# Performance work log

Hardware: AMD Instinct MI355X
Metric: run time of the kernel (lower is better)

## Reference

```python
import jax, jax.numpy as jnp
import numpy as np

DIM = 384
HEADS = 12
HEAD_DIM = DIM // HEADS
WIN = (2, 7, 7)
NW_TOK = WIN[0] * WIN[1] * WIN[2]  # 98
SCALE = HEAD_DIM ** -0.5


def _relative_position_index():
    d = np.arange(WIN[0]); h = np.arange(WIN[1]); w = np.arange(WIN[2])
    coords = np.stack(np.meshgrid(d, h, w, indexing='ij'))  # [3,D,H,W]
    cf = coords.reshape(3, -1)  # [3, NW_TOK]
    rel = cf[:, :, None] - cf[:, None, :]  # [3, N, N]
    rel = rel.transpose(1, 2, 0).astype(np.int64)
    rel[:, :, 0] += WIN[0] - 1
    rel[:, :, 1] += WIN[1] - 1
    rel[:, :, 2] += WIN[2] - 1
    rel[:, :, 0] *= (2 * WIN[1] - 1) * (2 * WIN[2] - 1)
    rel[:, :, 1] *= 2 * WIN[2] - 1
    return rel.sum(-1)  # [NW_TOK, NW_TOK]


def setup_inputs() -> dict:
    key = jax.random.key(0)
    ks = jax.random.split(key, 6)
    B_, N = 1024, NW_TOK + 1
    nW = 64
    table_len = (2 * WIN[0] - 1) * (2 * WIN[1] - 1) * (2 * WIN[2] - 1)  # 507
    x = jax.random.normal(ks[0], (B_, N, DIM), dtype=jnp.float32)
    mask = jax.random.normal(ks[1], (nW, NW_TOK, NW_TOK), dtype=jnp.float32)
    W_qkv = jax.random.normal(ks[2], (DIM, 3 * DIM), dtype=jnp.float32) * 0.02
    rpb_table = jax.random.normal(ks[3], (table_len, HEADS), dtype=jnp.float32) * 0.02
    W_proj = jax.random.normal(ks[4], (DIM, DIM), dtype=jnp.float32) * 0.02
    b_proj = jnp.zeros((DIM,), dtype=jnp.float32)
    rpi = jnp.asarray(_relative_position_index(), dtype=jnp.int32)
    return {"x": x, "mask": mask, "W_qkv": W_qkv, "rpb_table": rpb_table,
            "W_proj": W_proj, "b_proj": b_proj, "rpi": rpi}


def reference(x, mask, W_qkv, rpb_table, W_proj, b_proj, rpi):
    B_, N, C = x.shape
    qkv = (x @ W_qkv).reshape(B_, N, 3, HEADS, HEAD_DIM)
    q, k, v = qkv[:, :, 0], qkv[:, :, 1], qkv[:, :, 2]  # [B_, N, H, hd]
    attn = jnp.einsum('bnhd,bmhd->bhnm', q * SCALE, k)  # [B_, H, N, N]
    # gathered relative position bias over non-class tokens, zero-padded for class token
    bias = rpb_table[rpi.reshape(-1)].reshape(NW_TOK, NW_TOK, HEADS).transpose(2, 0, 1)
    bias_full = jnp.pad(bias, ((0, 0), (1, 0), (1, 0)))  # [H, N, N]
    attn = attn + bias_full[None]
    nW = mask.shape[0]
    mask_full = jnp.pad(mask, ((0, 0), (1, 0), (1, 0)))  # [nW, N, N]
    attn = attn.reshape(B_ // nW, nW, HEADS, N, N) + mask_full[None, :, None]
    attn = attn.reshape(B_, HEADS, N, N)
    attn = jax.nn.softmax(attn, axis=-1)
    out = jnp.einsum('bhnm,bmhd->bnhd', attn, v).reshape(B_, N, C)
    out = out @ W_proj + b_proj
    return out[:, 1:], out[:, :1]
```

## Files before the change

kernel.cpp:

```cpp
#include <hip/hip_runtime.h>
#include <hip/hip_bf16.h>
#include <cstddef>
#include <cstdint>


using bf16 = __hip_bfloat16;
typedef short v8s __attribute__((ext_vector_type(8)));
typedef short v4s __attribute__((ext_vector_type(4)));
typedef float v4f __attribute__((ext_vector_type(4)));

static constexpr int    NTOK   = 99;
static constexpr int    CDIM   = 384;
static constexpr int    NHEAD  = 12;
static constexpr int    NROWS  = 101376;
static constexpr size_t PLANE  = (size_t)NROWS * 32;
static constexpr float  SCALEF = 0.17677669529663687f;

__device__ __forceinline__ v4f mfma16x16x32(v8s a, v8s b, v4f c) {
  return __builtin_amdgcn_mfma_f32_16x16x32_bf16(a, b, c, 0, 0, 0);
}
__device__ __forceinline__ short f2bf(float f) {
  bf16 h = __float2bfloat16(f);
  return *reinterpret_cast<short*>(&h);
}
__device__ __forceinline__ float bf2f(short s) {
  bf16 h = *reinterpret_cast<bf16*>(&s);
  return __bfloat162float(h);
}

#if defined(__has_builtin)
#if __has_builtin(__builtin_amdgcn_global_load_lds)
#define HAS_GLL 1
#endif
#endif
#ifndef HAS_GLL
#define HAS_GLL 0
#endif

__device__ __forceinline__ void gload_lds16(const bf16* gsrc, bf16* ldst, int lane) {
#if HAS_GLL
  __builtin_amdgcn_global_load_lds(
      (const __attribute__((address_space(1))) void*)gsrc,
      (__attribute__((address_space(3))) void*)ldst, 16, 0, 0);
#else
  *(v8s*)(ldst + lane * 8) = *(const v8s*)gsrc;
#endif
}

static constexpr size_t WT_QKV_OFF = 0;
static constexpr size_t WT_P_OFF   = 884736;
static constexpr size_t BIAS_OFF   = 884736 + 294912;
static constexpr size_t COMMON_END = 1650096;
static constexpr size_t O_WS_OFF   = COMMON_END;
static constexpr size_t WS_MID     = O_WS_OFF + (size_t)NROWS * 384 * 2;
static constexpr size_t BMF_OFF    = COMMON_END;
static constexpr size_t BMF_BYTES  = (size_t)64 * NHEAD * 7 * 7 * 64 * 4 * 2;
static constexpr size_t QKV_OFF    = BMF_OFF + BMF_BYTES;
static constexpr size_t WS_FULL    = QKV_OFF + (size_t)NROWS * 1152 * 2;
static constexpr size_t XB_OFF     = WS_FULL;
static constexpr size_t WS_FULL2   = XB_OFF + (size_t)NROWS * 384 * 2;

static constexpr int PREP_BASE = 1152 * 384 + 384 * 384 + NHEAD * 99 * 99;
static constexpr int PREP_BMF2 = 64 * 112 * 112;
static constexpr int PREP_XB   = NROWS * 384 / 8;

__global__ void prep_kernel(const float* __restrict__ Wqkv, const float* __restrict__ Wproj,
                            const float* __restrict__ rpb,  const int* __restrict__ rpi,
                            const float* __restrict__ mask, const float* __restrict__ x,
                            bf16* __restrict__ WtQKV, bf16* __restrict__ WtP,
                            float* __restrict__ BIAS, bf16* __restrict__ BMF,
                            bf16* __restrict__ xb, int do_bmf, int do_xb)
{
  int idx = blockIdx.x * 256 + threadIdx.x;
  if (idx < 1152 * 384) {
    int c = idx / 384, k = idx - c * 384;
    WtQKV[idx] = __float2bfloat16(Wqkv[k * 1152 + c]);
  } else if (idx < 1152 * 384 + 384 * 384) {
    int j = idx - 1152 * 384;
    int c = j / 384, k = j - c * 384;
    WtP[j] = __float2bfloat16(Wproj[k * 384 + c]);
  } else if (idx < PREP_BASE) {
    int j = idx - (1152 * 384 + 384 * 384);
    int h = j / (99 * 99), r = j % (99 * 99);
    int nn = r / 99, mm = r % 99;
    float v = 0.f;
    if (nn > 0 && mm > 0) v = rpb[rpi[(nn - 1) * 98 + (mm - 1)] * NHEAD + h];
    BIAS[j] = v;
  } else if (do_bmf && idx < PREP_BASE + PREP_BMF2) {
    int j2  = idx - PREP_BASE;
    int col = j2 % 112;
    int r2  = j2 / 112;
    int row = r2 % 112;
    int wi  = r2 / 112;
    int w = row >> 4, g = (row >> 2) & 3, jj = row & 3;
    int t = col >> 4, li = col & 15, lane = g * 16 + li;
    bool in = (row >= 1 && row <= 98 && col >= 1 && col <= 98);
    int tix = 0; float mval = 0.f;
    if (in) {
      tix  = rpi[(row - 1) * 98 + (col - 1)];
      mval = mask[((size_t)wi * 98 + (row - 1)) * 98 + (col - 1)];
    }
    size_t base = (((size_t)wi * NHEAD * 7 + w) * 7 + t) * 256 + lane * 4 + jj;
    #pragma unroll
    for (int h = 0; h < NHEAD; ++h) {
      float v = in ? (rpb[tix * NHEAD + h] + mval) : 0.f;
      BMF[base + (size_t)h * 12544] = __float2bfloat16(v);
    }
  } else if (do_xb && idx >= PREP_BASE + PREP_BMF2 &&
             idx < PREP_BASE + PREP_BMF2 + PREP_XB) {
    int j3 = idx - (PREP_BASE + PREP_BMF2);
    size_t off = (size_t)j3 * 8;
    v4f x0 = *(const v4f*)(x + off);
    v4f x1 = *(const v4f*)(x + off + 4);
    v8s f;
    #pragma unroll
    for (int j = 0; j < 4; ++j) { f[j] = f2bf(x0[j]); f[j + 4] = f2bf(x1[j]); }
    *(v8s*)(xb + off) = f;
  }
}

static constexpr int Q2_BUF  = 40960;
static constexpr int Q2_AOFF = 24576;
static constexpr int CSTG_LD = 104;

__global__ __launch_bounds__(512)
void k_qkv2(const bf16* __restrict__ xb, const bf16* __restrict__ WtQKV,
            bf16* __restrict__ qkv2)
{
  __shared__ __align__(16) char smem[2 * Q2_BUF];
  bf16* C_stg = (bf16*)(smem);

  const int tid  = threadIdx.x;
  const int wave = tid >> 6;
  const int wm   = wave >> 2;
  const int wn   = wave & 3;
  const int lane = tid & 63;
  const int g    = lane >> 4;
  const int li   = lane & 15;
  const int tile = (blockIdx.x & 7) * 594 + (blockIdx.x >> 3);
  const int R0   = (tile / 6) * 128;
  const int CN   = (tile % 6) * 192;

  v4f acc[4][3];
  #pragma unroll
  for (int mi = 0; mi < 4; ++mi)
    #pragma unroll
    for (int ni = 0; ni < 3; ++ni) acc[mi][ni] = (v4f){0.f, 0.f, 0.f, 0.f};

  auto stage = [&](int kc, int buf) {
    const int k0 = kc * 64;
    bf16* Bl = (bf16*)(smem + buf * Q2_BUF);
    bf16* Al = (bf16*)(smem + buf * Q2_BUF + Q2_AOFF);
    #pragma unroll
    for (int p = 0; p < 3; ++p) {
      int q = wave * 3 + p;
      int row = q * 8 + (lane >> 3);
      int c = (lane & 7) ^ (row & 7);
      gload_lds16(WtQKV + (size_t)(CN + row) * 384 + k0 + c * 8, Bl + q * 512, lane);
    }
    #pragma unroll
    for (int p = 0; p < 2; ++p) {
      int q = wave * 2 + p;
      int row = q * 8 + (lane >> 3);
      int c = (lane & 7) ^ (row & 7);
      gload_lds16(xb + (size_t)(R0 + row) * 384 + k0 + c * 8, Al + q * 512, lane);
    }
  };

  stage(0, 0);
  for (int kc = 0; kc < 6; ++kc) {
    if (kc < 5) {
      stage(kc + 1, (kc + 1) & 1);
      asm volatile("s_waitcnt vmcnt(5)" ::: "memory");
    } else {
      asm volatile("s_waitcnt vmcnt(0)" ::: "memory");
    }
    __builtin_amdgcn_s_barrier();
    __builtin_amdgcn_sched_barrier(0);
    const bf16* Bl = (const bf16*)(smem + (kc & 1) * Q2_BUF);
    const bf16* Al = (const bf16*)(smem + (kc & 1) * Q2_BUF + Q2_AOFF);
    #pragma unroll
    for (int ks = 0; ks < 2; ++ks) {
      v8s af[4], bfr[3];
      #pragma unroll
      for (int mi = 0; mi < 4; ++mi) {
        int arow = wm * 64 + mi * 16 + li;
        int sc   = (4 * ks + g) ^ (arow & 7);
        af[mi] = *(const v8s*)(Al + arow * 64 + sc * 8);
      }
      #pragma unroll
      for (int ni = 0; ni < 3; ++ni) {
        int brow = wn * 48 + ni * 16 + li;
        int sc   = (4 * ks + g) ^ (brow & 7);
        bfr[ni] = *(const v8s*)(Bl + brow * 64 + sc * 8);
      }
      #pragma unroll
      for (int mi = 0; mi < 4; ++mi)
        #pragma unroll
        for (int ni = 0; ni < 3; ++ni)
          acc[mi][ni] = mfma16x16x32(af[mi], bfr[ni], acc[mi][ni]);
    }
    __builtin_amdgcn_sched_barrier(0);
    __builtin_amdgcn_s_barrier();
  }

  const float scale = (CN < 384) ? SCALEF : 1.f;
  const int r_ep = tid >> 2, d8 = tid & 3;
  #pragma unroll
  for (int half = 0; half < 2; ++half) {
    __syncthreads();
    if ((wn >> 1) == half) {
      #pragma unroll
      for (int mi = 0; mi < 4; ++mi)
        #pragma unroll
        for (int ni = 0; ni < 3; ++ni)
          #pragma unroll
          for (int j = 0; j < 4; ++j)
            C_stg[(wm * 64 + mi * 16 + g * 4 + j) * CSTG_LD + (wn & 1) * 48 + ni * 16 + li] =
                __float2bfloat16(acc[mi][ni][j] * scale);
    }
    __syncthreads();
    #pragma unroll
    for (int cidx = 0; cidx < 3; ++cidx) {
      int c_global = CN + half * 96 + cidx * 32;
      int seg = c_global / 384, hh = (c_global % 384) >> 5;
      bf16* plane = qkv2 + (size_t)(hh * 3 + seg) * PLANE;
      v8s val = *(const v8s*)(C_stg + r_ep * CSTG_LD + cidx * 32 + d8 * 8);
      *(v8s*)(plane + (size_t)(R0 + r_ep) * 32 + d8 * 8) = val;
    }
  }
}

static constexpr int GQB_OFF  = 0;
static constexpr int GQA_OFF  = 24576;
static constexpr int GQ_LDS2  = GQA_OFF + 128 * 72 * 2;

__global__ __launch_bounds__(512)
void k_qkv(const float* __restrict__ x, const bf16* __restrict__ WtQKV,
           bf16* __restrict__ qkv2)
{
  __shared__ __align__(16) char smem[GQ_LDS2];
  bf16* B_lds = (bf16*)(smem + GQB_OFF);
  bf16* A_lds = (bf16*)(smem + GQA_OFF);
  bf16* C_stg = (bf16*)(smem);

  const int tid  = threadIdx.x;
  const int wave = tid >> 6;
  const int wm   = wave >> 2;
  const int wn   = wave & 3;
  const int lane = tid & 63;
  const int g    = lane >> 4;
  const int li   = lane & 15;
  const int tile = (blockIdx.x & 7) * 594 + (blockIdx.x >> 3);
  const int R0   = (tile / 6) * 128;
  const int CN   = (tile % 6) * 192;

  const int arr = tid >> 3, ak8 = tid & 7;

  v4f acc[4][3];
  #pragma unroll
  for (int mi = 0; mi < 4; ++mi)
    #pragma unroll
    for (int ni = 0; ni < 3; ++ni) acc[mi][ni] = (v4f){0.f, 0.f, 0.f, 0.f};

  v4f areg[2][2];
  auto load_areg = [&](int kc) {
    const int k0 = kc * 64;
    #pragma unroll
    for (int p = 0; p < 2; ++p) {
      const float* src = x + (size_t)(R0 + arr + p * 64) * 384 + k0 + ak8 * 8;
      areg[p][0] = *(const v4f*)(src);
      areg[p][1] = *(const v4f*)(src + 4);
    }
  };
  auto write_alds = [&]() {
    #pragma unroll
    for (int p = 0; p < 2; ++p) {
      v8s f;
      #pragma unroll
      for (int j = 0; j < 4; ++j) { f[j] = f2bf(areg[p][0][j]); f[j + 4] = f2bf(areg[p][1][j]); }
      *(v8s*)(A_lds + (arr + p * 64) * 72 + ak8 * 8) = f;
    }
  };

  load_areg(0);

  for (int kc = 0; kc < 6; ++kc) {
    const int k0 = kc * 64;
    write_alds();
    #pragma unroll
    for (int p = 0; p < 3; ++p) {
      int q   = wave * 3 + p;
      int row = q * 8 + (lane >> 3);
      int c   = (lane & 7) ^ (row & 7);
      const bf16* gsrc = WtQKV + (size_t)(CN + row) * 384 + k0 + c * 8;
      gload_lds16(gsrc, B_lds + q * 512, lane);
    }
    if (kc < 5) load_areg(kc + 1);
    __syncthreads();
    #pragma unroll
    for (int ks = 0; ks < 2; ++ks) {
      v8s af[4], bfr[3];
      #pragma unroll
      for (int mi = 0; mi < 4; ++mi)
        af[mi] = *(const v8s*)(A_lds + (wm * 64 + mi * 16 + li) * 72 + ks * 32 + g * 8);
      #pragma unroll
      for (int ni = 0; ni < 3; ++ni) {
        int brow = wn * 48 + ni * 16 + li;
        int sc   = (g + 4 * ks) ^ (brow & 7);
        bfr[ni]  = *(const v8s*)(B_lds + brow * 64 + sc * 8);
      }
      #pragma unroll
      for (int mi = 0; mi < 4; ++mi)
        #pragma unroll
        for (int ni = 0; ni < 3; ++ni)
          acc[mi][ni] = mfma16x16x32(af[mi], bfr[ni], acc[mi][ni]);
    }
    __syncthreads();
  }

  const float scale = (CN < 384) ? SCALEF : 1.f;
  const int r_ep = tid >> 2, d8 = tid & 3;
  #pragma unroll
  for (int half = 0; half < 2; ++half) {
    __syncthreads();
    if ((wn >> 1) == half) {
      #pragma unroll
      for (int mi = 0; mi < 4; ++mi)
        #pragma unroll
        for (int ni = 0; ni < 3; ++ni)
          #pragma unroll
          for (int j = 0; j < 4; ++j)
            C_stg[(wm * 64 + mi * 16 + g * 4 + j) * CSTG_LD + (wn & 1) * 48 + ni * 16 + li] =
                __float2bfloat16(acc[mi][ni][j] * scale);
    }
    __syncthreads();
    #pragma unroll
    for (int cidx = 0; cidx < 3; ++cidx) {
      int c_global = CN + half * 96 + cidx * 32;
      int seg = c_global / 384, hh = (c_global % 384) >> 5;
      bf16* plane = qkv2 + (size_t)(hh * 3 + seg) * PLANE;
      v8s val = *(const v8s*)(C_stg + r_ep * CSTG_LD + cidx * 32 + d8 * 8);
      *(v8s*)(plane + (size_t)(R0 + r_ep) * 32 + d8 * 8) = val;
    }
  }
}

static constexpr int A_VT_LD = 136;
static constexpr int A_P_LD  = 136;
static constexpr int A_OFF_V = 0;
static constexpr int A_OFF_P = A_OFF_V + 32 * A_VT_LD * 2;
static constexpr int A_LDS   = A_OFF_P + 112 * A_P_LD * 2;

__global__ __launch_bounds__(448)
void k_attn(const bf16* __restrict__ BMF, bf16* __restrict__ qkv2)
{
  __shared__ __align__(16) char smem[A_LDS];
  bf16* vT_lds = (bf16*)(smem + A_OFF_V);
  bf16* P_lds  = (bf16*)(smem + A_OFF_P);

  const int b    = blockIdx.x;
  const int h0   = blockIdx.y * 3;
  const int tid  = threadIdx.x;
  const int wave = tid >> 6;
  const int lane = tid & 63;
  const int g    = lane >> 4;
  const int li   = lane & 15;
  const int wi   = b & 63;

  for (int z = tid; z < 32 * 29; z += 448)
    vT_lds[(z / 29) * A_VT_LD + 99 + (z % 29)] = __float2bfloat16(0.f);
  for (int z = tid; z < 112 * 29; z += 448)
    P_lds[(z / 29) * A_P_LD + 99 + (z % 29)] = __float2bfloat16(0.f);

  const int r = tid >> 2, l4 = tid & 3;
  const size_t voff = ((size_t)b * NTOK + ((r > 98) ? 98 : r)) * 32 + l4 * 8;

  const int qrow = (16 * wave + li > 98) ? 98 : 16 * wave + li;
  const size_t qoff = ((size_t)b * NTOK + qrow) * 32 + g * 8;
  size_t koff[7];
  #pragma unroll
  for (int t = 0; t < 7; ++t) {
    int krow = 16 * t + li; if (krow > 98) krow = 98;
    koff[t] = ((size_t)b * NTOK + krow) * 32 + g * 8;
  }

  {
    v8s pv = *(const v8s*)(qkv2 + (size_t)(h0 * 3 + 2) * PLANE + voff);
    if (r < NTOK) {
      #pragma unroll
      for (int e = 0; e < 8; ++e)
        *(short*)(vT_lds + (l4 * 8 + e) * A_VT_LD + r) = pv[e];
    }
  }
  __syncthreads();

  v4f oaccs[3][2];

  #pragma unroll
  for (int hi = 0; hi < 3; ++hi) {
    const int h = h0 + hi;
    v8s nv;
    if (hi < 2) nv = *(const v8s*)(qkv2 + (size_t)(h * 3 + 5) * PLANE + voff);

    const bf16* kp = qkv2 + (size_t)(h * 3 + 1) * PLANE;
    v8s kf[7];
    #pragma unroll
    for (int t = 0; t < 7; ++t) kf[t] = *(const v8s*)(kp + koff[t]);
    v8s qf = *(const v8s*)(qkv2 + (size_t)(h * 3 + 0) * PLANE + qoff);

    const bf16* bmb = BMF + ((size_t)((wi * NHEAD + h) * 7 + wave) * 7) * 256;
    v4s bmr[7];
    #pragma unroll
    for (int t = 0; t < 7; ++t)
      bmr[t] = *(const v4s*)(bmb + t * 256 + lane * 4);

    v4f sacc[7];
    #pragma unroll
    for (int t = 0; t < 7; ++t) {
      v4f z = (v4f){0.f, 0.f, 0.f, 0.f};
      sacc[t] = mfma16x16x32(qf, kf[t], z);
    }
    #pragma unroll
    for (int t = 0; t < 7; ++t) {
      int col = 16 * t + li;
      #pragma unroll
      for (int j = 0; j < 4; ++j) {
        float s = sacc[t][j];
        if (col >= NTOK) s = -1e30f;
        else             s += bf2f(bmr[t][j]);
        sacc[t][j] = s;
      }
    }
    float linv[4];
    #pragma unroll
    for (int j = 0; j < 4; ++j) {
      float m = -1e30f;
      #pragma unroll
      for (int t = 0; t < 7; ++t) m = fmaxf(m, sacc[t][j]);
      m = fmaxf(m, __shfl_xor(m, 1));
      m = fmaxf(m, __shfl_xor(m, 2));
      m = fmaxf(m, __shfl_xor(m, 4));
      m = fmaxf(m, __shfl_xor(m, 8));
      float l = 0.f;
      #pragma unroll
      for (int t = 0; t < 7; ++t) {
        float p = __expf(sacc[t][j] - m);
        sacc[t][j] = p;
        l += p;
      }
      l += __shfl_xor(l, 1);
      l += __shfl_xor(l, 2);
      l += __shfl_xor(l, 4);
      l += __shfl_xor(l, 8);
      linv[j] = 1.f / l;
      int row = 16 * wave + g * 4 + j;
      #pragma unroll
      for (int t = 0; t < 7; ++t) {
        int col = 16 * t + li;
        if (col < NTOK) P_lds[row * A_P_LD + col] = __float2bfloat16(sacc[t][j]);
      }
    }
    v4f oacc[2];
    oacc[0] = (v4f){0.f, 0.f, 0.f, 0.f};
    oacc[1] = (v4f){0.f, 0.f, 0.f, 0.f};
    #pragma unroll
    for (int ks = 0; ks < 4; ++ks) {
      v8s ap = *(const v8s*)(P_lds + (16 * wave + li) * A_P_LD + ks * 32 + g * 8);
      #pragma unroll
      for (int t = 0; t < 2; ++t) {
        v8s bv = *(const v8s*)(vT_lds + (16 * t + li) * A_VT_LD + ks * 32 + g * 8);
        oacc[t] = mfma16x16x32(ap, bv, oacc[t]);
      }
    }
    #pragma unroll
    for (int t = 0; t < 2; ++t)
      #pragma unroll
      for (int j = 0; j < 4; ++j)
        oaccs[hi][t][j] = oacc[t][j] * linv[j];

    __syncthreads();
    if (hi < 2) {
      if (r < NTOK) {
        #pragma unroll
        for (int e = 0; e < 8; ++e)
          *(short*)(vT_lds + (l4 * 8 + e) * A_VT_LD + r) = nv[e];
      }
      __syncthreads();
    }
  }

  #pragma unroll
  for (int hi = 0; hi < 3; ++hi) {
    bf16* oplane = qkv2 + (size_t)((h0 + hi) * 3) * PLANE;
    #pragma unroll
    for (int t = 0; t < 2; ++t)
      #pragma unroll
      for (int j = 0; j < 4; ++j) {
        int row = 16 * wave + g * 4 + j;
        if (row < NTOK)
          oplane[((size_t)b * NTOK + row) * 32 + 16 * t + li] =
              __float2bfloat16(oaccs[hi][t][j]);
      }
  }
}

__global__ __launch_bounds__(512)
void k2_proj2(const bf16* __restrict__ O_src, const bf16* __restrict__ WtP,
              const float* __restrict__ bproj, float* __restrict__ out)
{
  __shared__ __align__(16) char smem[2 * Q2_BUF];

  const int tid  = threadIdx.x;
  const int wave = tid >> 6;
  const int wm   = wave >> 2;
  const int wn   = wave & 3;
  const int lane = tid & 63;
  const int g    = lane >> 4;
  const int li   = lane & 15;
  const int tile = (blockIdx.x & 7) * 198 + (blockIdx.x >> 3);
  const int R0   = (tile >> 1) * 128;
  const int CN   = (tile & 1) * 192;

  v4f acc[4][3];
  #pragma unroll
  for (int mi = 0; mi < 4; ++mi)
    #pragma unroll
    for (int ni = 0; ni < 3; ++ni) acc[mi][ni] = (v4f){0.f, 0.f, 0.f, 0.f};

  auto stage = [&](int kc, int buf) {
    const int k0 = kc * 64;
    bf16* Wl = (bf16*)(smem + buf * Q2_BUF);
    bf16* Ol = (bf16*)(smem + buf * Q2_BUF + Q2_AOFF);
    #pragma unroll
    for (int p = 0; p < 3; ++p) {
      int q = wave * 3 + p;
      int row = q * 8 + (lane >> 3);
      int c = (lane & 7) ^ (row & 7);
      gload_lds16(WtP + (size_t)(CN + row) * CDIM + k0 + c * 8, Wl + q * 512, lane);
    }
    #pragma unroll
    for (int p = 0; p < 2; ++p) {
      int q = wave * 2 + p;
      int row = q * 8 + (lane >> 3);
      int c = (lane & 7) ^ (row & 7);
      int kk = k0 + c * 8, hh = kk >> 5, d = kk & 31;
      gload_lds16(O_src + (size_t)(hh * 3) * PLANE + (size_t)(R0 + row) * 32 + d,
                  Ol + q * 512, lane);
    }
  };

  stage(0, 0);
  for (int kc = 0; kc < 6; ++kc) {
    if (kc < 5) {
      stage(kc + 1, (kc + 1) & 1);
      asm volatile("s_waitcnt vmcnt(5)" ::: "memory");
    } else {
      asm volatile("s_waitcnt vmcnt(0)" ::: "memory");
    }
    __builtin_amdgcn_s_barrier();
    __builtin_amdgcn_sched_barrier(0);
    const bf16* Wl = (const bf16*)(smem + (kc & 1) * Q2_BUF);
    const bf16* Ol = (const bf16*)(smem + (kc & 1) * Q2_BUF + Q2_AOFF);
    #pragma unroll
    for (int ks = 0; ks < 2; ++ks) {
      v8s af[4], bfr[3];
      #pragma unroll
      for (int mi = 0; mi < 4; ++mi) {
        int arow = wm * 64 + mi * 16 + li;
        int sc   = (4 * ks + g) ^ (arow & 7);
        af[mi] = *(const v8s*)(Ol + arow * 64 + sc * 8);
      }
      #pragma unroll
      for (int ni = 0; ni < 3; ++ni) {
        int brow = wn * 48 + ni * 16 + li;
        int sc   = (4 * ks + g) ^ (brow & 7);
        bfr[ni] = *(const v8s*)(Wl + brow * 64 + sc * 8);
      }
      #pragma unroll
      for (int mi = 0; mi < 4; ++mi)
        #pragma unroll
        for (int ni = 0; ni < 3; ++ni)
          acc[mi][ni] = mfma16x16x32(af[mi], bfr[ni], acc[mi][ni]);
    }
    __builtin_amdgcn_sched_barrier(0);
    __builtin_amdgcn_s_barrier();
  }

  const size_t OUT2 = (size_t)1024 * 98 * CDIM;
  #pragma unroll
  for (int mi = 0; mi < 4; ++mi)
    #pragma unroll
    for (int ni = 0; ni < 3; ++ni) {
      int col = CN + wn * 48 + ni * 16 + li;
      float bb = bproj[col];
      #pragma unroll
      for (int j = 0; j < 4; ++j) {
        int rr = R0 + wm * 64 + mi * 16 + g * 4 + j;
        int b = rr / 99, n = rr - b * 99;
        float v = acc[mi][ni][j] + bb;
        if (n == 0) out[OUT2 + (size_t)b * CDIM + col] = v;
        else        out[((size_t)b * 98 + (n - 1)) * CDIM + col] = v;
      }
    }
}

static constexpr int K2_LD   = 72;
static constexpr int K2_OFFW = 0;
static constexpr int K2_OFFO = 192 * K2_LD * 2;
static constexpr int K2_LDS  = K2_OFFO + 128 * K2_LD * 2;

__global__ __launch_bounds__(512)
void k2_proj(const bf16* __restrict__ O_src, const bf16* __restrict__ WtP,
             const float* __restrict__ bproj, float* __restrict__ out)
{
  __shared__ __align__(16) char smem[K2_LDS];
  bf16* W_lds = (bf16*)(smem + K2_OFFW);
  bf16* O_lds = (bf16*)(smem + K2_OFFO);

  const int tid  = threadIdx.x;
  const int wave = tid >> 6;
  const int wm   = wave >> 2;
  const int wn   = wave & 3;
  const int lane = tid & 63;
  const int g    = lane >> 4;
  const int li   = lane & 15;
  const int tile = (blockIdx.x & 7) * 198 + (blockIdx.x >> 3);
  const int R0   = (tile >> 1) * 128;
  const int CN   = (tile & 1) * 192;

  v4f acc[4][3];
  #pragma unroll
  for (int mi = 0; mi < 4; ++mi)
    #pragma unroll
    for (int ni = 0; ni < 3; ++ni) acc[mi][ni] = (v4f){0.f, 0.f, 0.f, 0.f};

  for (int kc = 0; kc < 6; ++kc) {
    const int k0 = kc * 64;
    #pragma unroll
    for (int p = 0; p < 3; ++p) {
      int it = tid + p * 512, rr = it >> 3, k8 = it & 7;
      *(v8s*)(W_lds + rr * K2_LD + k8 * 8) =
          *(const v8s*)(WtP + (size_t)(CN + rr) * CDIM + k0 + k8 * 8);
    }
    #pragma unroll
    for (int p = 0; p < 2; ++p) {
      int it = tid + p * 512, rr = it >> 3, k8 = it & 7;
      *(v8s*)(O_lds + rr * K2_LD + k8 * 8) =
          *(const v8s*)(O_src + (size_t)(R0 + rr) * 384 + k0 + k8 * 8);
    }
    __syncthreads();
    #pragma unroll
    for (int ks = 0; ks < 2; ++ks) {
      v8s af[4], bfr[3];
      #pragma unroll
      for (int mi = 0; mi < 4; ++mi)
        af[mi] = *(const v8s*)(O_lds + (wm * 64 + mi * 16 + li) * K2_LD + ks * 32 + g * 8);
      #pragma unroll
      for (int ni = 0; ni < 3; ++ni)
        bfr[ni] = *(const v8s*)(W_lds + (wn * 48 + ni * 16 + li) * K2_LD + ks * 32 + g * 8);
      #pragma unroll
      for (int mi = 0; mi < 4; ++mi)
        #pragma unroll
        for (int ni = 0; ni < 3; ++ni)
          acc[mi][ni] = mfma16x16x32(af[mi], bfr[ni], acc[mi][ni]);
    }
    __syncthreads();
  }

  const size_t OUT2 = (size_t)1024 * 98 * CDIM;
  #pragma unroll
  for (int mi = 0; mi < 4; ++mi)
    #pragma unroll
    for (int ni = 0; ni < 3; ++ni) {
      int col = CN + wn * 48 + ni * 16 + li;
      float bb = bproj[col];
      #pragma unroll
      for (int j = 0; j < 4; ++j) {
        int rr = R0 + wm * 64 + mi * 16 + g * 4 + j;
        int b = rr / 99, n = rr - b * 99;
        float v = acc[mi][ni][j] + bb;
        if (n == 0) out[OUT2 + (size_t)b * CDIM + col] = v;
        else        out[((size_t)b * 98 + (n - 1)) * CDIM + col] = v;
      }
    }
}

static constexpr int QK_LD = 40;
static constexpr int VT_LD = 136;
static constexpr int P_LD  = 136;
static constexpr int WS_LD = 104;
static constexpr int K1_OFF_Q = 0;
static constexpr int K1_OFF_K = K1_OFF_Q + 112 * QK_LD * 2;
static constexpr int K1_OFF_V = K1_OFF_K + 112 * QK_LD * 2;
static constexpr int K1_OFF_P = K1_OFF_V + 32  * VT_LD * 2;
static constexpr int K1_OFF_W = K1_OFF_P + 112 * P_LD  * 2;
static constexpr int K1_LDS   = K1_OFF_W + 96 * WS_LD * 2;

__global__ __launch_bounds__(512)
void k1_attn(const float* __restrict__ x, const float* __restrict__ mask,
             const float* __restrict__ BIAS, const bf16* __restrict__ WtQKV,
             bf16* __restrict__ O_ws)
{
  __shared__ __align__(16) char smem[K1_LDS];
  bf16* q_lds  = (bf16*)(smem + K1_OFF_Q);
  bf16* k_lds  = (bf16*)(smem + K1_OFF_K);
  bf16* vT_lds = (bf16*)(smem + K1_OFF_V);
  bf16* P_lds  = (bf16*)(smem + K1_OFF_P);
  bf16* w_lds  = (bf16*)(smem + K1_OFF_W);

  const int b    = blockIdx.x;
  const int tid  = threadIdx.x;
  const int wave = tid >> 6;
  const int lane = tid & 63;
  const int g    = lane >> 4;
  const int li   = lane & 15;
  const int wi   = b & 63;

  v8s afr[12];
  if (wave < 7) {
    int arow = 16 * wave + li; if (arow > 98) arow = 98;
    const float* xb = x + ((size_t)b * NTOK + arow) * CDIM + g * 8;
    #pragma unroll
    for (int s = 0; s < 12; ++s) {
      v4f x0 = *(const v4f*)(xb + s * 32);
      v4f x1 = *(const v4f*)(xb + s * 32 + 4);
      v8s f;
      #pragma unroll
      for (int j = 0; j < 4; ++j) { f[j] = f2bf(x0[j]); f[j + 4] = f2bf(x1[j]); }
      afr[s] = f;
    }
  }

  for (int h = 0; h < NHEAD; ++h) {
    v4f qacc[6];
    #pragma unroll
    for (int t = 0; t < 6; ++t) qacc[t] = (v4f){0.f, 0.f, 0.f, 0.f};
    #pragma unroll
    for (int c4 = 0; c4 < 4; ++c4) {
      for (int idx = tid; idx < 96 * 12; idx += 512) {
        int rr = idx / 12, ch = idx - rr * 12;
        int cg = (rr < 32) ? (h * 32 + rr)
               : (rr < 64) ? (CDIM + h * 32 + rr - 32)
                           : (2 * CDIM + h * 32 + rr - 64);
        *(v8s*)(w_lds + rr * WS_LD + ch * 8) =
            *(const v8s*)(WtQKV + (size_t)cg * CDIM + c4 * 96 + ch * 8);
      }
      __syncthreads();
      if (wave < 7) {
        #pragma unroll
        for (int ss = 0; ss < 3; ++ss) {
          const int s = c4 * 3 + ss;
          #pragma unroll
          for (int t = 0; t < 6; ++t) {
            v8s bw = *(const v8s*)(w_lds + (16 * t + li) * WS_LD + ss * 32 + g * 8);
            qacc[t] = mfma16x16x32(afr[s], bw, qacc[t]);
          }
        }
      }
      __syncthreads();
    }
    if (wave < 7) {
      #pragma unroll
      for (int t = 0; t < 6; ++t) {
        #pragma unroll
        for (int j = 0; j < 4; ++j) {
          int row = 16 * wave + g * 4 + j;
          int col = 16 * (t & 1) + li;
          float v = qacc[t][j];
          if (t < 2)      q_lds[row * QK_LD + col] = __float2bfloat16(v * SCALEF);
          else if (t < 4) k_lds[row * QK_LD + col] = __float2bfloat16(v);
          else            vT_lds[col * VT_LD + row] = __float2bfloat16(v);
        }
      }
    }
    vT_lds[(tid >> 4) * VT_LD + 112 + (tid & 15)] = __float2bfloat16(0.f);
    __syncthreads();

    if (wave < 7) {
      v8s aq = *(const v8s*)(q_lds + (16 * wave + li) * QK_LD + g * 8);
      v4f sacc[7];
      #pragma unroll
      for (int t = 0; t < 7; ++t) {
        v8s bk = *(const v8s*)(k_lds + (16 * t + li) * QK_LD + g * 8);
        v4f z = (v4f){0.f, 0.f, 0.f, 0.f};
        sacc[t] = mfma16x16x32(aq, bk, z);
      }
      #pragma unroll
      for (int t = 0; t < 7; ++t) {
        int col = 16 * t + li;
        #pragma unroll
        for (int j = 0; j < 4; ++j) {
          int row = 16 * wave + g * 4 + j;
          float s = sacc[t][j];
          if (col >= NTOK) s = -1e30f;
          else if (row < NTOK) {
            s += BIAS[(h * NTOK + row) * NTOK + col];
            if (row > 0 && col > 0)
              s += mask[((size_t)wi * 98 + (row - 1)) * 98 + (col - 1)];
          }
          sacc[t][j] = s;
        }
      }
      float linv[4];
      #pragma unroll
      for (int j = 0; j < 4; ++j) {
        float m = -1e30f;
        #pragma unroll
        for (int t = 0; t < 7; ++t) m = fmaxf(m, sacc[t][j]);
        m = fmaxf(m, __shfl_xor(m, 1));
        m = fmaxf(m, __shfl_xor(m, 2));
        m = fmaxf(m, __shfl_xor(m, 4));
        m = fmaxf(m, __shfl_xor(m, 8));
        float l = 0.f;
        #pragma unroll
        for (int t = 0; t < 7; ++t) {
          float p = __expf(sacc[t][j] - m);
          sacc[t][j] = p;
          l += p;
        }
        l += __shfl_xor(l, 1);
        l += __shfl_xor(l, 2);
        l += __shfl_xor(l, 4);
        l += __shfl_xor(l, 8);
        linv[j] = 1.f / l;
        int row = 16 * wave + g * 4 + j;
        #pragma unroll
        for (int t = 0; t < 7; ++t)
          P_lds[row * P_LD + 16 * t + li] = __float2bfloat16(sacc[t][j]);
        P_lds[row * P_LD + 112 + li] = __float2bfloat16(0.f);
      }
      v4f oacc[2];
      oacc[0] = (v4f){0.f, 0.f, 0.f, 0.f};
      oacc[1] = (v4f){0.f, 0.f, 0.f, 0.f};
      #pragma unroll
      for (int ks = 0; ks < 4; ++ks) {
        v8s ap = *(const v8s*)(P_lds + (16 * wave + li) * P_LD + ks * 32 + g * 8);
        #pragma unroll
        for (int t = 0; t < 2; ++t) {
          v8s bv = *(const v8s*)(vT_lds + (16 * t + li) * VT_LD + ks * 32 + g * 8);
          oacc[t] = mfma16x16x32(ap, bv, oacc[t]);
        }
      }
      #pragma unroll
      for (int t = 0; t < 2; ++t) {
        #pragma unroll
        for (int j = 0; j < 4; ++j) {
          int row = 16 * wave + g * 4 + j;
          if (row < NTOK)
            O_ws[((size_t)b * 99 + row) * CDIM + h * 32 + 16 * t + li] =
                __float2bfloat16(oacc[t][j] * linv[j]);
        }
      }
    }
    __syncthreads();
  }
}

static constexpr int M_O_LD = 392;
static constexpr int M_OFF_O = 0;
static constexpr int M_OFF_Q = M_OFF_O + 99  * M_O_LD * 2;
static constexpr int M_OFF_K = M_OFF_Q + 112 * QK_LD * 2;
static constexpr int M_OFF_V = M_OFF_K + 112 * QK_LD * 2;
static constexpr int M_OFF_P = M_OFF_V + 32  * VT_LD * 2;
static constexpr int M_OFF_W = M_OFF_P + 112 * P_LD  * 2;
static constexpr int M_LDS   = M_OFF_W + 96 * WS_LD * 2;

__global__ __launch_bounds__(512)
void fused_mono(const float* __restrict__ x, const float* __restrict__ mask,
                const float* __restrict__ bproj, const float* __restrict__ BIAS,
                const bf16* __restrict__ WtQKV, const bf16* __restrict__ WtP,
                float* __restrict__ out)
{
  __shared__ __align__(16) char smem[M_LDS];
  bf16* O_lds  = (bf16*)(smem + M_OFF_O);
  bf16* q_lds  = (bf16*)(smem + M_OFF_Q);
  bf16* k_lds  = (bf16*)(smem + M_OFF_K);
  bf16* vT_lds = (bf16*)(smem + M_OFF_V);
  bf16* P_lds  = (bf16*)(smem + M_OFF_P);
  bf16* w_lds  = (bf16*)(smem + M_OFF_W);

  const int b    = blockIdx.x;
  const int tid  = threadIdx.x;
  const int wave = tid >> 6;
  const int lane = tid & 63;
  const int g    = lane >> 4;
  const int li   = lane & 15;
  const int wi   = b & 63;

  v8s afr[12];
  if (wave < 7) {
    int arow = 16 * wave + li; if (arow > 98) arow = 98;
    const float* xb = x + ((size_t)b * NTOK + arow) * CDIM + g * 8;
    #pragma unroll
    for (int s = 0; s < 12; ++s) {
      v4f x0 = *(const v4f*)(xb + s * 32);
      v4f x1 = *(const v4f*)(xb + s * 32 + 4);
      v8s f;
      #pragma unroll
      for (int j = 0; j < 4; ++j) { f[j] = f2bf(x0[j]); f[j + 4] = f2bf(x1[j]); }
      afr[s] = f;
    }
  }

  for (int h = 0; h < NHEAD; ++h) {
    v4f qacc[6];
    #pragma unroll
    for (int t = 0; t < 6; ++t) qacc[t] = (v4f){0.f, 0.f, 0.f, 0.f};
    #pragma unroll
    for (int c4 = 0; c4 < 4; ++c4) {
      for (int idx = tid; idx < 96 * 12; idx += 512) {
        int rr = idx / 12, ch = idx - rr * 12;
        int cg = (rr < 32) ? (h * 32 + rr)
               : (rr < 64) ? (CDIM + h * 32 + rr - 32)
                           : (2 * CDIM + h * 32 + rr - 64);
        *(v8s*)(w_lds + rr * WS_LD + ch * 8) =
            *(const v8s*)(WtQKV + (size_t)cg * CDIM + c4 * 96 + ch * 8);
      }
      __syncthreads();
      if (wave < 7) {
        #pragma unroll
        for (int ss = 0; ss < 3; ++ss) {
          const int s = c4 * 3 + ss;
          #pragma unroll
          for (int t = 0; t < 6; ++t) {
            v8s bw = *(const v8s*)(w_lds + (16 * t + li) * WS_LD + ss * 32 + g * 8);
            qacc[t] = mfma16x16x32(afr[s], bw, qacc[t]);
          }
        }
      }
      __syncthreads();
    }
    if (wave < 7) {
      #pragma unroll
      for (int t = 0; t < 6; ++t) {
        #pragma unroll
        for (int j = 0; j < 4; ++j) {
          int row = 16 * wave + g * 4 + j;
          int col = 16 * (t & 1) + li;
          float v = qacc[t][j];
          if (t < 2)      q_lds[row * QK_LD + col] = __float2bfloat16(v * SCALEF);
          else if (t < 4) k_lds[row * QK_LD + col] = __float2bfloat16(v);
          else            vT_lds[col * VT_LD + row] = __float2bfloat16(v);
        }
      }
    }
    vT_lds[(tid >> 4) * VT_LD + 112 + (tid & 15)] = __float2bfloat16(0.f);
    __syncthreads();

    if (wave < 7) {
      v8s aq = *(const v8s*)(q_lds + (16 * wave + li) * QK_LD + g * 8);
      v4f sacc[7];
      #pragma unroll
      for (int t = 0; t < 7; ++t) {
        v8s bk = *(const v8s*)(k_lds + (16 * t + li) * QK_LD + g * 8);
        v4f z = (v4f){0.f, 0.f, 0.f, 0.f};
        sacc[t] = mfma16x16x32(aq, bk, z);
      }
      #pragma unroll
      for (int t = 0; t < 7; ++t) {
        int col = 16 * t + li;
        #pragma unroll
        for (int j = 0; j < 4; ++j) {
          int row = 16 * wave + g * 4 + j;
          float s = sacc[t][j];
          if (col >= NTOK) s = -1e30f;
          else if (row < NTOK) {
            s += BIAS[(h * NTOK + row) * NTOK + col];
            if (row > 0 && col > 0)
              s += mask[((size_t)wi * 98 + (row - 1)) * 98 + (col - 1)];
          }
          sacc[t][j] = s;
        }
      }
      float linv[4];
      #pragma unroll
      for (int j = 0; j < 4; ++j) {
        float m = -1e30f;
        #pragma unroll
        for (int t = 0; t < 7; ++t) m = fmaxf(m, sacc[t][j]);
        m = fmaxf(m, __shfl_xor(m, 1));
        m = fmaxf(m, __shfl_xor(m, 2));
        m = fmaxf(m, __shfl_xor(m, 4));
        m = fmaxf(m, __shfl_xor(m, 8));
        float l = 0.f;
        #pragma unroll
        for (int t = 0; t < 7; ++t) {
          float p = __expf(sacc[t][j] - m);
          sacc[t][j] = p;
          l += p;
        }
        l += __shfl_xor(l, 1);
        l += __shfl_xor(l, 2);
        l += __shfl_xor(l, 4);
        l += __shfl_xor(l, 8);
        linv[j] = 1.f / l;
        int row = 16 * wave + g * 4 + j;
        #pragma unroll
        for (int t = 0; t < 7; ++t)
          P_lds[row * P_LD + 16 * t + li] = __float2bfloat16(sacc[t][j]);
        P_lds[row * P_LD + 112 + li] = __float2bfloat16(0.f);
      }
      v4f oacc[2];
      oacc[0] = (v4f){0.f, 0.f, 0.f, 0.f};
      oacc[1] = (v4f){0.f, 0.f, 0.f, 0.f};
      #pragma unroll
      for (int ks = 0; ks < 4; ++ks) {
        v8s ap = *(const v8s*)(P_lds + (16 * wave + li) * P_LD + ks * 32 + g * 8);
        #pragma unroll
        for (int t = 0; t < 2; ++t) {
          v8s bv = *(const v8s*)(vT_lds + (16 * t + li) * VT_LD + ks * 32 + g * 8);
          oacc[t] = mfma16x16x32(ap, bv, oacc[t]);
        }
      }
      #pragma unroll
      for (int t = 0; t < 2; ++t) {
        #pragma unroll
        for (int j = 0; j < 4; ++j) {
          int row = 16 * wave + g * 4 + j;
          if (row < NTOK)
            O_lds[row * M_O_LD + h * 32 + 16 * t + li] =
                __float2bfloat16(oacc[t][j] * linv[j]);
        }
      }
    }
    __syncthreads();
  }

  const size_t OUT2 = (size_t)1024 * 98 * CDIM;
  const int orow_clamped = (16 * wave + li > 98) ? 98 : 16 * wave + li;
  for (int cc = 0; cc < 4; ++cc) {
    v4f pacc[6];
    #pragma unroll
    for (int t = 0; t < 6; ++t) pacc[t] = (v4f){0.f, 0.f, 0.f, 0.f};
    for (int c4 = 0; c4 < 4; ++c4) {
      for (int idx = tid; idx < 96 * 12; idx += 512) {
        int rr = idx / 12, ch = idx - rr * 12;
        *(v8s*)(w_lds + rr * WS_LD + ch * 8) =
            *(const v8s*)(WtP + ((size_t)(cc * 96 + rr)) * CDIM + c4 * 96 + ch * 8);
      }
      __syncthreads();
      if (wave < 7) {
        #pragma unroll
        for (int ss = 0; ss < 3; ++ss) {
          const int s = c4 * 3 + ss;
          v8s ao = *(const v8s*)(O_lds + orow_clamped * M_O_LD + s * 32 + g * 8);
          #pragma unroll
          for (int t = 0; t < 6; ++t) {
            v8s bw = *(const v8s*)(w_lds + (16 * t + li) * WS_LD + ss * 32 + g * 8);
            pacc[t] = mfma16x16x32(ao, bw, pacc[t]);
          }
        }
      }
      __syncthreads();
    }
    if (wave < 7) {
      #pragma unroll
      for (int t = 0; t < 6; ++t) {
        #pragma unroll
        for (int j = 0; j < 4; ++j) {
          int row = 16 * wave + g * 4 + j;
          if (row < NTOK) {
            int col = cc * 96 + 16 * t + li;
            float v = pacc[t][j] + bproj[col];
            if (row == 0) out[OUT2 + (size_t)b * CDIM + col] = v;
            else          out[((size_t)b * 98 + (row - 1)) * CDIM + col] = v;
          }
        }
      }
    }
  }
}

extern "C" void kernel_launch(void* const* d_in, const int* in_sizes, int n_in,
                              void* d_out, int out_size, void* d_ws, size_t ws_size,
                              hipStream_t stream) {
  const float* x     = (const float*)d_in[0];
  const float* mask  = (const float*)d_in[1];
  const float* Wqkv  = (const float*)d_in[2];
  const float* rpb   = (const float*)d_in[3];
  const float* Wproj = (const float*)d_in[4];
  const float* bproj = (const float*)d_in[5];
  const int*   rpi   = (const int*)d_in[6];

  bf16*  WtQKV = (bf16*)((char*)d_ws + WT_QKV_OFF);
  bf16*  WtP   = (bf16*)((char*)d_ws + WT_P_OFF);
  float* BIAS  = (float*)((char*)d_ws + BIAS_OFF);
  bf16*  BMF   = (bf16*)((char*)d_ws + BMF_OFF);
  bf16*  xbuf  = (bf16*)((char*)d_ws + XB_OFF);

  const bool full2 = (ws_size >= WS_FULL2);
  const bool full  = (ws_size >= WS_FULL);
  int prep_items = PREP_BASE;
  if (full)  prep_items += PREP_BMF2;
  if (full2) prep_items += PREP_XB;
  prep_kernel<<<(prep_items + 255) / 256, 256, 0, stream>>>(
      Wqkv, Wproj, rpb, rpi, mask, x, WtQKV, WtP, BIAS, BMF, xbuf,
      full ? 1 : 0, full2 ? 1 : 0);

  if (full) {
    bf16* qkv2 = (bf16*)((char*)d_ws + QKV_OFF);
    if (full2) k_qkv2<<<792 * 6, 512, 0, stream>>>(xbuf, WtQKV, qkv2);
    else       k_qkv<<<792 * 6, 512, 0, stream>>>(x, WtQKV, qkv2);
    k_attn<<<dim3(1024, 4), 448, 0, stream>>>(BMF, qkv2);
    k2_proj2<<<792 * 2, 512, 0, stream>>>(qkv2, WtP, bproj, (float*)d_out);
  } else if (ws_size >= WS_MID) {
    bf16* O_ws = (bf16*)((char*)d_ws + O_WS_OFF);
    k1_attn<<<1024, 512, 0, stream>>>(x, mask, BIAS, WtQKV, O_ws);
    k2_proj<<<792 * 2, 512, 0, stream>>>(O_ws, WtP, bproj, (float*)d_out);
  } else {
    fused_mono<<<1024, 512, 0, stream>>>(x, mask, bproj, BIAS, WtQKV, WtP,
                                         (float*)d_out);
  }
}
```

Before: 442.3 us.

## Prefetch next head's Q/K/V in attention kernel and fold padding mask into bias

Result: faster. 422.8 us (-4.4%).

```diff
diff --git a/kernel.cpp b/kernel.cpp
--- a/kernel.cpp
+++ b/kernel.cpp
@@ -103,7 +103,9 @@
     size_t base = (((size_t)wi * NHEAD * 7 + w) * 7 + t) * 256 + lane * 4 + jj;
     #pragma unroll
     for (int h = 0; h < NHEAD; ++h) {
-      float v = in ? (rpb[tix * NHEAD + h] + mval) : 0.f;
+      float v;
+      if (col > 98)  v = -1e30f;
+      else           v = in ? (rpb[tix * NHEAD + h] + mval) : 0.f;
       BMF[base + (size_t)h * 12544] = __float2bfloat16(v);
     }
   } else if (do_xb && idx >= PREP_BASE + PREP_BMF2 &&
@@ -360,7 +362,7 @@
   bf16* P_lds  = (bf16*)(smem + A_OFF_P);
 
   const int b    = blockIdx.x;
-  const int h0   = blockIdx.y * 3;
+  const int h0   = blockIdx.y * 6;
   const int tid  = threadIdx.x;
   const int wave = tid >> 6;
   const int lane = tid & 63;
@@ -368,46 +370,42 @@
   const int li   = lane & 15;
   const int wi   = b & 63;
 
-  for (int z = tid; z < 32 * 29; z += 448)
-    vT_lds[(z / 29) * A_VT_LD + 99 + (z % 29)] = __float2bfloat16(0.f);
-  for (int z = tid; z < 112 * 29; z += 448)
-    P_lds[(z / 29) * A_P_LD + 99 + (z % 29)] = __float2bfloat16(0.f);
-
   const int r = tid >> 2, l4 = tid & 3;
   const size_t voff = ((size_t)b * NTOK + ((r > 98) ? 98 : r)) * 32 + l4 * 8;
 
   const int qrow = (16 * wave + li > 98) ? 98 : 16 * wave + li;
   const size_t qoff = ((size_t)b * NTOK + qrow) * 32 + g * 8;
-  size_t koff[7];
+  int koff[7];
   #pragma unroll
   for (int t = 0; t < 7; ++t) {
     int krow = 16 * t + li; if (krow > 98) krow = 98;
-    koff[t] = ((size_t)b * NTOK + krow) * 32 + g * 8;
-  }
-
+    koff[t] = (b * NTOK + krow) * 32 + g * 8;
+  }
+
+  v8s pv = *(const v8s*)(qkv2 + (size_t)(h0 * 3 + 2) * PLANE + voff);
+
+  for (int z = tid; z < A_LDS / 16; z += 448)
+    *(v8s*)(smem + z * 16) = (v8s){0, 0, 0, 0, 0, 0, 0, 0};
+  __syncthreads();
+
+  if (r < NTOK) {
+    #pragma unroll
+    for (int e = 0; e < 8; ++e)
+      *(short*)(vT_lds + (l4 * 8 + e) * A_VT_LD + r) = pv[e];
+  }
+
+  v8s kf[7], qf;
   {
-    v8s pv = *(const v8s*)(qkv2 + (size_t)(h0 * 3 + 2) * PLANE + voff);
-    if (r < NTOK) {
-      #pragma unroll
-      for (int e = 0; e < 8; ++e)
-        *(short*)(vT_lds + (l4 * 8 + e) * A_VT_LD + r) = pv[e];
-    }
+    const bf16* kp = qkv2 + (size_t)(h0 * 3 + 1) * PLANE;
+    #pragma unroll
+    for (int t = 0; t < 7; ++t) kf[t] = *(const v8s*)(kp + koff[t]);
+    qf = *(const v8s*)(qkv2 + (size_t)(h0 * 3) * PLANE + qoff);
   }
   __syncthreads();
 
-  v4f oaccs[3][2];
-
   #pragma unroll
-  for (int hi = 0; hi < 3; ++hi) {
+  for (int hi = 0; hi < 6; ++hi) {
     const int h = h0 + hi;
-    v8s nv;
-    if (hi < 2) nv = *(const v8s*)(qkv2 + (size_t)(h * 3 + 5) * PLANE + voff);
-
-    const bf16* kp = qkv2 + (size_t)(h * 3 + 1) * PLANE;
-    v8s kf[7];
-    #pragma unroll
-    for (int t = 0; t < 7; ++t) kf[t] = *(const v8s*)(kp + koff[t]);
-    v8s qf = *(const v8s*)(qkv2 + (size_t)(h * 3 + 0) * PLANE + qoff);
 
     const bf16* bmb = BMF + ((size_t)((wi * NHEAD + h) * 7 + wave) * 7) * 256;
     v4s bmr[7];
@@ -421,17 +419,22 @@
       v4f z = (v4f){0.f, 0.f, 0.f, 0.f};
       sacc[t] = mfma16x16x32(qf, kf[t], z);
     }
-    #pragma unroll
-    for (int t = 0; t < 7; ++t) {
-      int col = 16 * t + li;
-      #pragma unroll
-      for (int j = 0; j < 4; ++j) {
-        float s = sacc[t][j];
-        if (col >= NTOK) s = -1e30f;
-        else             s += bf2f(bmr[t][j]);
-        sacc[t][j] = s;
-      }
-    }
+
+    v8s nv;
+    if (hi < 5) {
+      const bf16* kp = qkv2 + (size_t)((h + 1) * 3 + 1) * PLANE;
+      #pragma unroll
+      for (int t = 0; t < 7; ++t) kf[t] = *(const v8s*)(kp + koff[t]);
+      qf = *(const v8s*)(qkv2 + (size_t)((h + 1) * 3) * PLANE + qoff);
+      nv = *(const v8s*)(qkv2 + (size_t)((h + 1) * 3 + 2) * PLANE + voff);
+    }
+
+    #pragma unroll
+    for (int t = 0; t < 7; ++t)
+      #pragma unroll
+      for (int j = 0; j < 4; ++j)
+        sacc[t][j] += bf2f(bmr[t][j]);
+
     float linv[4];
     #pragma unroll
     for (int j = 0; j < 4; ++j) {
@@ -456,10 +459,8 @@
       linv[j] = 1.f / l;
       int row = 16 * wave + g * 4 + j;
       #pragma unroll
-      for (int t = 0; t < 7; ++t) {
-        int col = 16 * t + li;
-        if (col < NTOK) P_lds[row * A_P_LD + col] = __float2bfloat16(sacc[t][j]);
-      }
+      for (int t = 0; t < 7; ++t)
+        P_lds[row * A_P_LD + 16 * t + li] = __float2bfloat16(sacc[t][j]);
     }
     v4f oacc[2];
     oacc[0] = (v4f){0.f, 0.f, 0.f, 0.f};
@@ -473,26 +474,7 @@
         oacc[t] = mfma16x16x32(ap, bv, oacc[t]);
       }
     }
-    #pragma unroll
-    for (int t = 0; t < 2; ++t)
-      #pragma unroll
-      for (int j = 0; j < 4; ++j)
-        oaccs[hi][t][j] = oacc[t][j] * linv[j];
-
-    __syncthreads();
-    if (hi < 2) {
-      if (r < NTOK) {
-        #pragma unroll
-        for (int e = 0; e < 8; ++e)
-          *(short*)(vT_lds + (l4 * 8 + e) * A_VT_LD + r) = nv[e];
-      }
-      __syncthreads();
-    }
-  }
-
-  #pragma unroll
-  for (int hi = 0; hi < 3; ++hi) {
-    bf16* oplane = qkv2 + (size_t)((h0 + hi) * 3) * PLANE;
+    bf16* oplane = qkv2 + (size_t)(h * 3) * PLANE;
     #pragma unroll
     for (int t = 0; t < 2; ++t)
       #pragma unroll
@@ -500,8 +482,18 @@
         int row = 16 * wave + g * 4 + j;
         if (row < NTOK)
           oplane[((size_t)b * NTOK + row) * 32 + 16 * t + li] =
-              __float2bfloat16(oaccs[hi][t][j]);
-      }
+              __float2bfloat16(oacc[t][j] * linv[j]);
+      }
+
+    __syncthreads();
+    if (hi < 5) {
+      if (r < NTOK) {
+        #pragma unroll
+        for (int e = 0; e < 8; ++e)
+          *(short*)(vT_lds + (l4 * 8 + e) * A_VT_LD + r) = nv[e];
+      }
+      __syncthreads();
+    }
   }
 }
 
@@ -1102,7 +1094,7 @@
     bf16* qkv2 = (bf16*)((char*)d_ws + QKV_OFF);
     if (full2) k_qkv2<<<792 * 6, 512, 0, stream>>>(xbuf, WtQKV, qkv2);
     else       k_qkv<<<792 * 6, 512, 0, stream>>>(x, WtQKV, qkv2);
-    k_attn<<<dim3(1024, 4), 448, 0, stream>>>(BMF, qkv2);
+    k_attn<<<dim3(1024, 2), 448, 0, stream>>>(BMF, qkv2);
     k2_proj2<<<792 * 2, 512, 0, stream>>>(qkv2, WtP, bproj, (float*)d_out);
   } else if (ws_size >= WS_MID) {
     bf16* O_ws = (bf16*)((char*)d_ws + O_WS_OFF);
```
